# Optimization experiments

Hardware: AMD Instinct MI355X
Metric: run time of the kernel (lower is better)

Reference implementation:

```python
import jax, jax.numpy as jnp
import numpy as np

DIM = 768
NUM_HEADS = 12
SMALLEST_RATIO = 0.25
LARGEST_RATIO = 1.0


def setup_inputs() -> dict:
    key = jax.random.key(0)
    k0, k1, k2 = jax.random.split(key, 3)
    B, N = 4, 2048
    x = jax.random.normal(k0, (B, N, DIM), dtype=jnp.float32)
    Wqkv = jax.random.normal(k1, (3 * DIM, DIM), dtype=jnp.float32) * 0.02
    bqkv = jnp.zeros((3 * DIM,), dtype=jnp.float32)
    Wproj = jax.random.normal(k2, (DIM, DIM), dtype=jnp.float32) * 0.02
    bproj = jnp.zeros((DIM,), dtype=jnp.float32)
    return {"x": x, "Wqkv": Wqkv, "bqkv": bqkv, "Wproj": Wproj, "bproj": bproj, "ratio": 1}


def reference(x, Wqkv, bqkv, Wproj, bproj, ratio):
    dc = int(ratio * DIM)
    # dynamic slimmable-width slicing: smallest/largest ratio take leading block,
    # intermediate ratios take trailing block
    if ratio == SMALLEST_RATIO or ratio == LARGEST_RATIO:
        wq, bq = Wqkv[: dc * 3, :dc], bqkv[: dc * 3]
        wp, bp = Wproj[:dc, :dc], bproj[:dc]
    else:
        wq, bq = Wqkv[-dc * 3 :, -dc:], bqkv[-dc * 3 :]
        wp, bp = Wproj[-dc:, -dc:], bproj[-dc:]
    B, N, C = x.shape
    hd = C // NUM_HEADS
    scale = (DIM // NUM_HEADS) ** -0.5  # set at init from full dim, not sliced C
    qkv = x @ wq.T + bq                               # [B, N, 3C]
    qkv = qkv.reshape(B, N, 3, NUM_HEADS, hd).transpose(2, 0, 3, 1, 4)  # [3,B,H,N,hd]
    q, k, v = qkv[0], qkv[1], qkv[2]
    attn = jax.nn.softmax(jnp.einsum("bhqd,bhkd->bhqk", q, k) * scale, axis=-1)
    out = jnp.einsum("bhqk,bhkd->bhqd", attn, v)      # [B,H,N,hd]
    out = out.transpose(0, 2, 1, 3).reshape(B, N, C)
    return out @ wp.T + bp
```

## Files before the change

kernel.cpp:

```cpp
#include <hip/hip_runtime.h>

typedef __bf16 bf16x8 __attribute__((ext_vector_type(8)));
typedef __bf16 bf16x2 __attribute__((ext_vector_type(2)));
typedef float  f32x4  __attribute__((ext_vector_type(4)));
typedef float  f32x16 __attribute__((ext_vector_type(16)));
typedef unsigned short u16;
typedef unsigned u32x2 __attribute__((ext_vector_type(2)));
typedef unsigned u32x4 __attribute__((ext_vector_type(4)));

__device__ __forceinline__ u16 f2bf(float f) {
  return __builtin_bit_cast(u16, (__bf16)f);
}
__device__ __forceinline__ unsigned pack2(float lo, float hi) {
  bf16x2 t;
  t[0] = (__bf16)lo; t[1] = (__bf16)hi;
  return __builtin_bit_cast(unsigned, t);
}

#define GLOAD16(g, l) __builtin_amdgcn_global_load_lds( \
    (__attribute__((address_space(1))) void*)(void*)(g), \
    (__attribute__((address_space(3))) void*)(l), 16, 0, 0)

#define QSCALE 0.18033688011112042f

__global__ __launch_bounds__(256) void cvt_bf16(const float* __restrict__ src,
                                                unsigned* __restrict__ dst, int n8) {
  int i = blockIdx.x * 256 + threadIdx.x;
  if (i >= n8) return;
  const float4* s = (const float4*)src + 2 * (size_t)i;
  float4 a = s[0], b = s[1];
  u32x4 o = {pack2(a.x, a.y), pack2(a.z, a.w), pack2(b.x, b.y), pack2(b.z, b.w)};
  *((u32x4*)dst + i) = o;
}

template<int EPI>
__global__ __launch_bounds__(256) void gemm_tn(
    const u16* __restrict__ A, const u16* __restrict__ B,
    const float* __restrict__ bias, float* __restrict__ outF,
    u16* __restrict__ qws, u16* __restrict__ kws, u16* __restrict__ vtws,
    int M, int N, int K) {
  __shared__ __align__(16) u16 As[8192];
  __shared__ __align__(16) u16 Bs[8192];
  const int tid = threadIdx.x;
  const int ln = tid & 63, wv = tid >> 6;
  const int wr = wv >> 1, wc = wv & 1;
  const int m0 = blockIdx.x * 128, n0 = blockIdx.y * 128;

  f32x4 acc[4][4] = {};

  const int c0 = tid, c1 = tid + 256;
  const int r0 = c0 >> 2, kc0 = ((c0 & 3) ^ ((r0 >> 1) & 3)) * 8;
  const int r1 = c1 >> 2, kc1 = ((c1 & 3) ^ ((r1 >> 1) & 3)) * 8;
  const u16* ag0 = A + (size_t)(m0 + r0) * K + kc0;
  const u16* ag1 = A + (size_t)(m0 + r1) * K + kc1;
  const u16* bg0 = B + (size_t)(n0 + r0) * K + kc0;
  const u16* bg1 = B + (size_t)(n0 + r1) * K + kc1;

  GLOAD16(ag0, As + wv * 512);
  GLOAD16(ag1, As + 2048 + wv * 512);
  GLOAD16(bg0, Bs + wv * 512);
  GLOAD16(bg1, Bs + 2048 + wv * 512);
  __syncthreads();

  int cur = 0;
  for (int k0 = 0; k0 < K; k0 += 32) {
    const int nxt = cur ^ 1;
    if (k0 + 32 < K) {
      GLOAD16(ag0 + k0 + 32, As + nxt * 4096 + wv * 512);
      GLOAD16(ag1 + k0 + 32, As + nxt * 4096 + 2048 + wv * 512);
      GLOAD16(bg0 + k0 + 32, Bs + nxt * 4096 + wv * 512);
      GLOAD16(bg1 + k0 + 32, Bs + nxt * 4096 + 2048 + wv * 512);
    }
    const u16* ab = As + cur * 4096;
    const u16* bb = Bs + cur * 4096;
    bf16x8 af[4], bfr[4];
#pragma unroll
    for (int i = 0; i < 4; ++i) {
      int ra = wr * 64 + i * 16 + (ln & 15);
      af[i] = *(const bf16x8*)(ab + ra * 32 + (((ln >> 4) ^ ((ra >> 1) & 3)) * 8));
      int rb = wc * 64 + i * 16 + (ln & 15);
      bfr[i] = *(const bf16x8*)(bb + rb * 32 + (((ln >> 4) ^ ((rb >> 1) & 3)) * 8));
    }
#pragma unroll
    for (int i = 0; i < 4; ++i)
#pragma unroll
      for (int j = 0; j < 4; ++j)
        acc[i][j] = __builtin_amdgcn_mfma_f32_16x16x32_bf16(af[i], bfr[j], acc[i][j], 0, 0, 0);
    __syncthreads();
    cur = nxt;
  }

  if (EPI == 1) {
#pragma unroll
    for (int j = 0; j < 4; ++j) {
      int col = n0 + wc * 64 + j * 16 + (ln & 15);
      float bj = bias[col];
#pragma unroll
      for (int i = 0; i < 4; ++i) {
        int mr = m0 + wr * 64 + i * 16 + ((ln >> 4) << 2);
#pragma unroll
        for (int r = 0; r < 4; ++r)
          outF[(size_t)(mr + r) * N + col] = acc[i][j][r] + bj;
      }
    }
  } else {
    const int s = n0 / 768;
#pragma unroll
    for (int j = 0; j < 4; ++j) {
      int col = n0 + wc * 64 + j * 16 + (ln & 15);
      float bj = bias[col];
      int ns = col - s * 768;
      int h = ns >> 6, d = ns & 63;
#pragma unroll
      for (int i = 0; i < 4; ++i) {
        int m = m0 + wr * 64 + i * 16 + ((ln >> 4) << 2);
        int b = m >> 11, iseq = m & 2047;
        size_t bh = (size_t)(b * 12 + h);
        if (s == 0) {
#pragma unroll
          for (int r = 0; r < 4; ++r)
            qws[(bh * 2048 + iseq + r) * 64 + d] = f2bf((acc[i][j][r] + bj) * QSCALE);
        } else if (s == 1) {
#pragma unroll
          for (int r = 0; r < 4; ++r)
            kws[(bh * 2048 + iseq + r) * 64 + d] = f2bf(acc[i][j][r] + bj);
        } else {
          u32x2 pk = {pack2(acc[i][j][0] + bj, acc[i][j][1] + bj),
                      pack2(acc[i][j][2] + bj, acc[i][j][3] + bj)};
          *(u32x2*)(vtws + (bh * 64 + d) * 2048 + iseq) = pk;
        }
      }
    }
  }
}

__global__ __launch_bounds__(256, 2) void attn_fa(
    const u16* __restrict__ qws, const u16* __restrict__ kws,
    const u16* __restrict__ vtws, u16* __restrict__ aows) {
  __shared__ __align__(16) u16 Ks[16384];
  __shared__ __align__(16) u16 Vs[16384];
  const int tid = threadIdx.x, ln = tid & 63, wv = tid >> 6;
  const int lq = ln & 31, hi = ln >> 5;
  const int qw = wv & 1;
  const int p  = wv >> 1;
  const int bh = blockIdx.y;
  const int q0 = blockIdx.x * 128 + qw * 64;
  const int kv0 = p * 1024;
  const size_t kbase = (size_t)bh * 2048 * 64;
  const size_t vbase = (size_t)bh * 64 * 2048;

  bf16x8 qf[2][4];
#pragma unroll
  for (int g = 0; g < 2; ++g) {
    const u16* qp = qws + kbase + (size_t)(q0 + g * 32 + lq) * 64 + hi * 8;
#pragma unroll
    for (int dc = 0; dc < 4; ++dc) qf[g][dc] = *(const bf16x8*)(qp + dc * 16);
  }

  const f32x16 zc = {};
  f32x16 o0[2] = {}, o1[2] = {};
  float ls0[2] = {0.f, 0.f}, ls1[2] = {0.f, 0.f};

  int offL[4], offH[4];
#pragma unroll
  for (int dc = 0; dc < 4; ++dc) {
    const int ch = dc * 2 + hi;
    offL[dc] = lq * 64 + ((ch ^ (lq & 7)) * 8);
    offH[dc] = (32 + lq) * 64 + ((ch ^ (lq & 7)) * 8);
  }

  const int lt = tid & 127;
  const int r0 = lt >> 3;
  const int pr0 = (r0 & ~12) | ((r0 & 4) << 1) | ((r0 & 8) >> 1);
  const int sc = ((lt & 7) ^ (r0 & 7)) * 8;
  const u16* kg = kws + kbase + (size_t)(kv0 + pr0) * 64 + sc;
  const u16* vg = vtws + vbase + (size_t)r0 * 2048 + kv0 + sc;
  u16* ksb = Ks + p * 8192;
  u16* vsb = Vs + p * 8192;
  const int sd = qw * 512;

#pragma unroll
  for (int j = 0; j < 4; ++j) {
    GLOAD16(kg + j * 1024, ksb + sd + j * 1024);
    GLOAD16(vg + (size_t)j * 32768, vsb + sd + j * 1024);
  }
  __syncthreads();

  int cur = 0;
  for (int kb = 0; kb < 1024; kb += 64) {
    const int nxt = cur ^ 1;
    if (kb + 64 < 1024) {
#pragma unroll
      for (int j = 0; j < 4; ++j) {
        GLOAD16(kg + (size_t)(kb + 64) * 64 + j * 1024, ksb + nxt * 4096 + sd + j * 1024);
        GLOAD16(vg + (kb + 64) + (size_t)j * 32768,     vsb + nxt * 4096 + sd + j * 1024);
      }
    }
    const u16* kbuf = ksb + cur * 4096;
    const u16* vbuf = vsb + cur * 4096;

    f32x16 s0[2], s1[2];
    {
      bf16x8 ka = *(const bf16x8*)(kbuf + offL[0]);
      bf16x8 kh = *(const bf16x8*)(kbuf + offH[0]);
      s0[0] = __builtin_amdgcn_mfma_f32_32x32x16_bf16(ka, qf[0][0], zc, 0, 0, 0);
      s0[1] = __builtin_amdgcn_mfma_f32_32x32x16_bf16(ka, qf[1][0], zc, 0, 0, 0);
      s1[0] = __builtin_amdgcn_mfma_f32_32x32x16_bf16(kh, qf[0][0], zc, 0, 0, 0);
      s1[1] = __builtin_amdgcn_mfma_f32_32x32x16_bf16(kh, qf[1][0], zc, 0, 0, 0);
    }
#pragma unroll
    for (int dc = 1; dc < 4; ++dc) {
      bf16x8 ka = *(const bf16x8*)(kbuf + offL[dc]);
      bf16x8 kh = *(const bf16x8*)(kbuf + offH[dc]);
      s0[0] = __builtin_amdgcn_mfma_f32_32x32x16_bf16(ka, qf[0][dc], s0[0], 0, 0, 0);
      s0[1] = __builtin_amdgcn_mfma_f32_32x32x16_bf16(ka, qf[1][dc], s0[1], 0, 0, 0);
      s1[0] = __builtin_amdgcn_mfma_f32_32x32x16_bf16(kh, qf[0][dc], s1[0], 0, 0, 0);
      s1[1] = __builtin_amdgcn_mfma_f32_32x32x16_bf16(kh, qf[1][dc], s1[1], 0, 0, 0);
    }

#pragma unroll
    for (int g = 0; g < 2; ++g) {
      float a0 = 0.f, a1 = 0.f;
#pragma unroll
      for (int r = 0; r < 16; ++r) {
        float e = __builtin_amdgcn_exp2f(s0[g][r]); s0[g][r] = e; a0 += e;
      }
#pragma unroll
      for (int r = 0; r < 16; ++r) {
        float e = __builtin_amdgcn_exp2f(s1[g][r]); s1[g][r] = e; a1 += e;
      }
      ls0[g] += a0; ls1[g] += a1;
    }

#pragma unroll
    for (int c = 0; c < 4; ++c) {
      bf16x8 va = *(const bf16x8*)(vbuf + offL[c]);
      bf16x8 vb = *(const bf16x8*)(vbuf + offH[c]);
#pragma unroll
      for (int g = 0; g < 2; ++g) {
        const f32x16& src = (c < 2) ? s0[g] : s1[g];
        const int base = (c & 1) * 8;
        u32x4 pw = {pack2(src[base + 0], src[base + 1]),
                    pack2(src[base + 2], src[base + 3]),
                    pack2(src[base + 4], src[base + 5]),
                    pack2(src[base + 6], src[base + 7])};
        bf16x8 pfrag = __builtin_bit_cast(bf16x8, pw);
        o0[g] = __builtin_amdgcn_mfma_f32_32x32x16_bf16(va, pfrag, o0[g], 0, 0, 0);
        o1[g] = __builtin_amdgcn_mfma_f32_32x32x16_bf16(vb, pfrag, o1[g], 0, 0, 0);
      }
    }
    __syncthreads();
    cur = nxt;
  }

  float lg[2];
#pragma unroll
  for (int g = 0; g < 2; ++g) {
    lg[g] = ls0[g] + ls1[g];
    lg[g] += __shfl_xor(lg[g], 32);
  }

  float* ex = (float*)(qw ? Vs : Ks);
  if (wv >= 2) {
    float* w = ex + ln * 66;
#pragma unroll
    for (int r = 0; r < 16; ++r) {
      w[r]      = o0[0][r];
      w[16 + r] = o1[0][r];
      w[32 + r] = o0[1][r];
      w[48 + r] = o1[1][r];
    }
    w[64] = lg[0]; w[65] = lg[1];
  }
  __syncthreads();
  if (wv < 2) {
    const float* w = ex + ln * 66;
#pragma unroll
    for (int r = 0; r < 16; ++r) {
      o0[0][r] += w[r];
      o1[0][r] += w[16 + r];
      o0[1][r] += w[32 + r];
      o1[1][r] += w[48 + r];
    }
    lg[0] += w[64]; lg[1] += w[65];

    const int b = bh / 12, h = bh % 12;
#pragma unroll
    for (int g = 0; g < 2; ++g) {
      const float rl = 1.0f / lg[g];
      u16* orow = aows + (size_t)(b * 2048 + q0 + g * 32 + lq) * 768 + h * 64;
#pragma unroll
      for (int t = 0; t < 4; ++t) {
        u32x2 pk0 = {pack2(o0[g][4 * t + 0] * rl, o0[g][4 * t + 1] * rl),
                     pack2(o0[g][4 * t + 2] * rl, o0[g][4 * t + 3] * rl)};
        u32x2 pk1 = {pack2(o1[g][4 * t + 0] * rl, o1[g][4 * t + 1] * rl),
                     pack2(o1[g][4 * t + 2] * rl, o1[g][4 * t + 3] * rl)};
        *(u32x2*)(orow + t * 8 + 4 * hi)      = pk0;
        *(u32x2*)(orow + 32 + t * 8 + 4 * hi) = pk1;
      }
    }
  }
}

extern "C" void kernel_launch(void* const* d_in, const int* in_sizes, int n_in,
                              void* d_out, int out_size, void* d_ws, size_t ws_size,
                              hipStream_t stream) {
  const float* x     = (const float*)d_in[0];
  const float* Wqkv  = (const float*)d_in[1];
  const float* bqkv  = (const float*)d_in[2];
  const float* Wproj = (const float*)d_in[3];
  const float* bproj = (const float*)d_in[4];
  float* out = (float*)d_out;

  u16* xb   = (u16*)d_ws;
  u16* wqb  = xb  + 6291456;
  u16* wpb  = wqb + 1769472;
  u16* qws  = wpb + 589824;
  u16* kws  = qws + 6291456;
  u16* vtws = kws + 6291456;
  u16* aows = vtws + 6291456;

  cvt_bf16<<<6291456 / 8 / 256, 256, 0, stream>>>(x, (unsigned*)xb, 6291456 / 8);
  cvt_bf16<<<1769472 / 8 / 256, 256, 0, stream>>>(Wqkv, (unsigned*)wqb, 1769472 / 8);
  cvt_bf16<<<589824 / 8 / 256, 256, 0, stream>>>(Wproj, (unsigned*)wpb, 589824 / 8);

  gemm_tn<0><<<dim3(64, 18), 256, 0, stream>>>(xb, wqb, bqkv, nullptr,
                                               qws, kws, vtws, 8192, 2304, 768);
  attn_fa<<<dim3(16, 48), 256, 0, stream>>>(qws, kws, vtws, aows);
  gemm_tn<1><<<dim3(64, 6), 256, 0, stream>>>(aows, wpb, bproj, out,
                                              nullptr, nullptr, nullptr,
                                              8192, 768, 768);
}
```

Measured before the change: 147.7 us.

## Read V fragments directly from global memory and drop V LDS staging

```diff
diff --git a/kernel.cpp b/kernel.cpp
--- a/kernel.cpp
+++ b/kernel.cpp
@@ -134,11 +134,12 @@
   }
 }
 
-__global__ __launch_bounds__(256, 2) void attn_fa(
+#define SWZ(v) (((v) & 32) | (((v) & 31) ^ (ln & 31)))
+__global__ __launch_bounds__(256, 3) void attn_fa(
     const u16* __restrict__ qws, const u16* __restrict__ kws,
     const u16* __restrict__ vtws, u16* __restrict__ aows) {
   __shared__ __align__(16) u16 Ks[16384];
-  __shared__ __align__(16) u16 Vs[16384];
+  __shared__ float Ls[256];
   const int tid = threadIdx.x, ln = tid & 63, wv = tid >> 6;
   const int lq = ln & 31, hi = ln >> 5;
   const int qw = wv & 1;
@@ -169,21 +170,19 @@
     offH[dc] = (32 + lq) * 64 + ((ch ^ (lq & 7)) * 8);
   }
 
+  const u16* vrow0 = vtws + vbase + (size_t)lq * 2048 + kv0;
+  const u16* vrow1 = vrow0 + (size_t)32 * 2048;
+
   const int lt = tid & 127;
   const int r0 = lt >> 3;
   const int pr0 = (r0 & ~12) | ((r0 & 4) << 1) | ((r0 & 8) >> 1);
   const int sc = ((lt & 7) ^ (r0 & 7)) * 8;
   const u16* kg = kws + kbase + (size_t)(kv0 + pr0) * 64 + sc;
-  const u16* vg = vtws + vbase + (size_t)r0 * 2048 + kv0 + sc;
   u16* ksb = Ks + p * 8192;
-  u16* vsb = Vs + p * 8192;
   const int sd = qw * 512;
 
 #pragma unroll
-  for (int j = 0; j < 4; ++j) {
-    GLOAD16(kg + j * 1024, ksb + sd + j * 1024);
-    GLOAD16(vg + (size_t)j * 32768, vsb + sd + j * 1024);
-  }
+  for (int j = 0; j < 4; ++j) GLOAD16(kg + j * 1024, ksb + sd + j * 1024);
   __syncthreads();
 
   int cur = 0;
@@ -191,13 +190,10 @@
     const int nxt = cur ^ 1;
     if (kb + 64 < 1024) {
 #pragma unroll
-      for (int j = 0; j < 4; ++j) {
+      for (int j = 0; j < 4; ++j)
         GLOAD16(kg + (size_t)(kb + 64) * 64 + j * 1024, ksb + nxt * 4096 + sd + j * 1024);
-        GLOAD16(vg + (kb + 64) + (size_t)j * 32768,     vsb + nxt * 4096 + sd + j * 1024);
-      }
     }
     const u16* kbuf = ksb + cur * 4096;
-    const u16* vbuf = vsb + cur * 4096;
 
     f32x16 s0[2], s1[2];
     {
@@ -232,10 +228,12 @@
       ls0[g] += a0; ls1[g] += a1;
     }
 
+    const u16* vp0 = vrow0 + kb;
+    const u16* vp1 = vrow1 + kb;
 #pragma unroll
     for (int c = 0; c < 4; ++c) {
-      bf16x8 va = *(const bf16x8*)(vbuf + offL[c]);
-      bf16x8 vb = *(const bf16x8*)(vbuf + offH[c]);
+      bf16x8 va = *(const bf16x8*)(vp0 + (c * 2 + hi) * 8);
+      bf16x8 vb = *(const bf16x8*)(vp1 + (c * 2 + hi) * 8);
 #pragma unroll
       for (int g = 0; g < 2; ++g) {
         const f32x16& src = (c < 2) ? s0[g] : s1[g];
@@ -260,29 +258,29 @@
     lg[g] += __shfl_xor(lg[g], 32);
   }
 
-  float* ex = (float*)(qw ? Vs : Ks);
-  if (wv >= 2) {
-    float* w = ex + ln * 66;
+  float* exO = (float*)Ks + qw * 4096 + ln * 64;
+  if (p == 1) {
 #pragma unroll
     for (int r = 0; r < 16; ++r) {
-      w[r]      = o0[0][r];
-      w[16 + r] = o1[0][r];
-      w[32 + r] = o0[1][r];
-      w[48 + r] = o1[1][r];
-    }
-    w[64] = lg[0]; w[65] = lg[1];
+      exO[SWZ(r)]      = o0[0][r];
+      exO[SWZ(16 + r)] = o1[0][r];
+      exO[SWZ(32 + r)] = o0[1][r];
+      exO[SWZ(48 + r)] = o1[1][r];
+    }
+    Ls[qw * 128 + ln * 2 + 0] = lg[0];
+    Ls[qw * 128 + ln * 2 + 1] = lg[1];
   }
   __syncthreads();
-  if (wv < 2) {
-    const float* w = ex + ln * 66;
+  if (p == 0) {
 #pragma unroll
     for (int r = 0; r < 16; ++r) {
-      o0[0][r] += w[r];
-      o1[0][r] += w[16 + r];
-      o0[1][r] += w[32 + r];
-      o1[1][r] += w[48 + r];
-    }
-    lg[0] += w[64]; lg[1] += w[65];
+      o0[0][r] += exO[SWZ(r)];
+      o1[0][r] += exO[SWZ(16 + r)];
+      o0[1][r] += exO[SWZ(32 + r)];
+      o1[1][r] += exO[SWZ(48 + r)];
+    }
+    lg[0] += Ls[qw * 128 + ln * 2 + 0];
+    lg[1] += Ls[qw * 128 + ln * 2 + 1];
 
     const int b = bh / 12, h = bh % 12;
 #pragma unroll
```

After: 217.5 us. +47.2%, slower.
